# Kernel optimization log

Measured on AMD Instinct MI355X. Metric: run time of the kernel, lower is better.

## Reference

```python
import jax, jax.numpy as jnp
import numpy as np

N, E, S, K, NB = 16384, 262144, 10, 64, 8
R_MAX, P_CUT, AVG_NEIGH = 5.0, 5, 16.0
L_OF_LM = np.array([0, 1, 1, 1, 2, 2, 2, 2, 2])  # l value of each of the 9 lm components
L_SLICES = [(0, 1), (1, 4), (4, 9)]               # lm ranges for l = 0,1,2
MLP_H = 16


def _sph(u):
    # real spherical harmonics up to l=2, e3nn 'component' normalization (sum_m Y_lm^2 = 2l+1)
    x, y, z = u[..., 0], u[..., 1], u[..., 2]
    s3, s15, s5 = np.float32(np.sqrt(3.0)), np.float32(np.sqrt(15.0)), np.float32(np.sqrt(5.0))
    return jnp.stack([
        jnp.ones_like(x),
        s3 * x, s3 * y, s3 * z,
        s15 * x * y, s15 * y * z, (s5 / 2) * (3 * z * z - 1), s15 * x * z, (s15 / 2) * (x * x - y * y),
    ], axis=-1)


def _radial(r):
    # Bessel radial basis with smooth polynomial cutoff envelope (p = P_CUT)
    u = r / R_MAX
    r_safe = jnp.where(r > 1e-9, r, 1.0)
    n = jnp.arange(1, NB + 1, dtype=r.dtype)
    bess = np.float32(np.sqrt(2.0 / R_MAX)) * jnp.sin(n * jnp.pi * u[:, None]) / r_safe[:, None]
    p = float(P_CUT)
    env = 1.0 - (p + 1) * (p + 2) / 2 * u**P_CUT + p * (p + 2) * u**(P_CUT + 1) - p * (p + 1) / 2 * u**(P_CUT + 2)
    env = jnp.where(u < 1.0, env, 0.0)
    return bess * env[:, None]  # [E, NB]


def setup_inputs() -> dict:
    key = jax.random.key(0)
    ks = jax.random.split(key, 16)
    positions = jax.random.uniform(ks[0], (N, 3), jnp.float32) * 4.0  # box so many edges fall inside r_max
    species = jax.random.randint(ks[1], (N,), 0, S)
    senders = jax.random.randint(ks[2], (E,), 0, N)
    receivers = jax.random.randint(ks[3], (E,), 0, N)
    shifts = jnp.zeros((E, 3), jnp.float32)
    W_embed = jax.random.normal(ks[4], (S, K), jnp.float32)
    W_rad = jax.random.normal(ks[5], (2, 3, NB, K), jnp.float32) * 0.3
    W_mix = jax.random.normal(ks[6], (2, 3, K, K), jnp.float32) / np.sqrt(K)
    W_prod = jax.random.normal(ks[7], (2, 3, 3, K), jnp.float32) * 0.1
    W_sc = jax.random.normal(ks[8], (2, S, 3, K, K), jnp.float32) / np.sqrt(K)
    W_ro0 = jax.random.normal(ks[9], (K,), jnp.float32) / np.sqrt(K)
    W_m1 = jax.random.normal(ks[10], (K, MLP_H), jnp.float32) / np.sqrt(K)
    b_m1 = jnp.zeros((MLP_H,), jnp.float32)
    W_m2 = jax.random.normal(ks[11], (MLP_H,), jnp.float32) / np.sqrt(MLP_H)
    return dict(positions=positions, shifts=shifts, species=species, senders=senders,
                receivers=receivers, W_embed=W_embed, W_rad=W_rad, W_mix=W_mix,
                W_prod=W_prod, W_sc=W_sc, W_ro0=W_ro0, W_m1=W_m1, b_m1=b_m1, W_m2=W_m2)


def reference(positions, shifts, species, senders, receivers, W_embed, W_rad, W_mix,
              W_prod, W_sc, W_ro0, W_m1, b_m1, W_m2):
    lm = jnp.asarray(L_OF_LM)
    onehot = jax.nn.one_hot(species, S, dtype=positions.dtype)
    # node embedding: scalars only -> feats [N, 9(lm), K]
    feats = jnp.zeros((N, 9, K), positions.dtype).at[:, 0, :].set(onehot @ W_embed)

    # edge geometry
    vec = positions[receivers] - positions[senders] + shifts           # [E, 3]
    r = jnp.linalg.norm(vec, axis=-1)                                  # [E]
    u_hat = vec / jnp.where(r > 1e-9, r, 1.0)[:, None]
    Y = _sph(u_hat)                                                     # [E, 9]
    rad = _radial(r)                                                    # [E, NB]

    energies = []
    for i in range(2):
        # interaction: radial-weighted SH messages from sender scalars, scatter-sum to receivers
        hs = feats[:, 0, :][senders]                                    # [E, K]
        Rl = jnp.einsum('eb,lbk->elk', rad, W_rad[i])[:, lm, :]         # [E, 9, K]
        msg = hs[:, None, :] * Y[:, :, None] * Rl                       # [E, 9, K]
        A = jax.ops.segment_sum(msg, receivers, num_segments=N) / AVG_NEIGH
        A = jnp.einsum('nmk,mkj->nmj', A, W_mix[i][lm])                 # per-l channel mixing

        # correlation-3 equivariant product basis (symmetric-contraction style)
        A0 = A[:, 0, :]
        inv = jnp.sum(A * A, axis=1)                                    # rotation-invariant [N, K]
        w1, w2, w3 = (W_prod[i, j][lm] for j in range(3))               # each [9, K]
        B = A * (w1[None] + w2[None] * A0[:, None, :] + w3[None] * inv[:, None, :])

        # species-dependent self-connection (linear of feats x node_attrs), per-l weights
        sc = jnp.concatenate([
            jnp.einsum('nmk,ns,skj->nmj', feats[:, st:en], onehot, W_sc[i, :, l])
            for l, (st, en) in enumerate(L_SLICES)], axis=1)
        feats = B + sc

        if i == 0:
            energies.append(feats[:, 0, :] @ W_ro0)                     # linear readout
        else:
            feats = feats.at[:, 1:, :].set(0.0)                         # last layer keeps 0e only
            energies.append(jax.nn.silu(feats[:, 0, :] @ W_m1 + b_m1) @ W_m2)

    return jnp.stack(energies, axis=1)  # [N, num_interactions]
```

## Files before the change

### kernel.cpp

```cpp
#include <hip/hip_runtime.h>

#define NN 16384
#define NE 262144
#define NSPEC 10
#define KC 64
#define MLPH 16
#define SEG 128
#define EPSG 2048
#define SC_NPB 16

typedef float v2f __attribute__((ext_vector_type(2)));

__device__ __forceinline__ float wave_reduce(float v) {
#pragma unroll
    for (int off = 32; off > 0; off >>= 1) v += __shfl_down(v, off, 64);
    return v;
}

__device__ __forceinline__ float f4c(const float4& v, int j) {
    const float* p = &v.x;
    return p[j];
}

__global__ void __launch_bounds__(1024) k_pre(
    const float* __restrict__ W_embed,
    const int* __restrict__ species,
    const int* __restrict__ receivers,
    int* __restrict__ eslot,
    unsigned short* __restrict__ cnt16,
    float4* __restrict__ h04) {
    __shared__ int cntL[NN];
    int t = threadIdx.x;
#pragma unroll
    for (int i = 0; i < 16; ++i) cntL[t + 1024 * i] = 0;
    __syncthreads();
    int ebase = blockIdx.x * EPSG;
#pragma unroll
    for (int j = 0; j < EPSG / 1024; ++j) {
        int e = ebase + j * 1024 + t;
        int r = receivers[e];
        eslot[e] = atomicAdd(&cntL[r], 1);
    }
    int gt = blockIdx.x * 1024 + t;
#pragma unroll
    for (int q = 0; q < 2; ++q) {
        int idx = gt * 2 + q;
        int n = idx >> 4, w = idx & 15;
        h04[idx] = reinterpret_cast<const float4*>(W_embed + species[n] * KC)[w];
    }
    __syncthreads();
    unsigned short* o = cnt16 + (size_t)blockIdx.x * NN;
#pragma unroll
    for (int i = 0; i < 16; ++i)
        o[t + 1024 * i] = (unsigned short)cntL[t + 1024 * i];
}

__global__ void __launch_bounds__(128) k_colscan(
    const unsigned short* __restrict__ cnt16,
    int* __restrict__ seg_base,
    int* __restrict__ count) {
    int r = blockIdx.x * 128 + threadIdx.x;
    int run = 0;
#pragma unroll 8
    for (int g = 0; g < SEG; ++g) {
        int c = cnt16[(size_t)g * NN + r];
        seg_base[(size_t)g * NN + r] = run;
        run += c;
    }
    count[r] = run;
}

__global__ void __launch_bounds__(1024) k_scan(
    const int* __restrict__ count, int* __restrict__ row_start,
    const int* __restrict__ species, int* __restrict__ nslot,
    int* __restrict__ sp_start) {
    __shared__ int lds[1024];
    __shared__ int itercnt[256 * NSPEC];
    __shared__ int spt[NSPEC];
    int t = threadIdx.x;
    int lane = t & 63;
    int w = t >> 6;
#pragma unroll
    for (int j = 0; j < 16; ++j) {
        int n = w * 1024 + j * 64 + lane;
        int sp = species[n];
#pragma unroll
        for (int s = 0; s < NSPEC; ++s) {
            unsigned long long mask = __ballot(sp == s);
            if (lane == 0) itercnt[(w * 16 + j) * NSPEC + s] = (int)__popcll(mask);
        }
    }
    int base = t * 16;
    int local[16];
    int ssum = 0;
#pragma unroll
    for (int b = 0; b < 16; ++b) { local[b] = count[base + b]; ssum += local[b]; }
    lds[t] = ssum;
    __syncthreads();
    for (int off = 1; off < 1024; off <<= 1) {
        int v = (t >= off) ? lds[t - off] : 0;
        __syncthreads();
        lds[t] += v;
        __syncthreads();
    }
    int run = lds[t] - ssum;
#pragma unroll
    for (int b = 0; b < 16; ++b) { row_start[base + b] = run; run += local[b]; }
    if (t == 1023) row_start[NN] = run;
    __syncthreads();
    if (w < NSPEC) {
        int s = w;
        int v0 = itercnt[(lane * 4 + 0) * NSPEC + s];
        int v1 = itercnt[(lane * 4 + 1) * NSPEC + s];
        int v2 = itercnt[(lane * 4 + 2) * NSPEC + s];
        int v3 = itercnt[(lane * 4 + 3) * NSPEC + s];
        int ls = v0 + v1 + v2 + v3;
        int inc = ls;
#pragma unroll
        for (int off = 1; off < 64; off <<= 1) {
            int v = __shfl_up(inc, off, 64);
            if (lane >= off) inc += v;
        }
        int exc = inc - ls;
        itercnt[(lane * 4 + 0) * NSPEC + s] = exc;
        itercnt[(lane * 4 + 1) * NSPEC + s] = exc + v0;
        itercnt[(lane * 4 + 2) * NSPEC + s] = exc + v0 + v1;
        itercnt[(lane * 4 + 3) * NSPEC + s] = exc + v0 + v1 + v2;
        if (lane == 63) spt[s] = inc;
    }
    __syncthreads();
    if (t == 0) {
        int r2 = 0;
        for (int s = 0; s < NSPEC; ++s) { sp_start[s] = r2; r2 += spt[s]; }
        sp_start[NSPEC] = r2;
    }
    __syncthreads();
#pragma unroll
    for (int j = 0; j < 16; ++j) {
        int n = w * 1024 + j * 64 + lane;
        int sp = species[n];
        int rank = 0;
#pragma unroll
        for (int s = 0; s < NSPEC; ++s) {
            unsigned long long mask = __ballot(sp == s);
            if (sp == s)
                rank = (int)__popcll(mask & ((1ull << lane) - 1ull));
        }
        nslot[n] = itercnt[(w * 16 + j) * NSPEC + sp] + rank;
    }
}

__global__ void k_geom(const float* __restrict__ pos,
                       const float* __restrict__ shifts,
                       const int* __restrict__ senders,
                       const int* __restrict__ receivers,
                       const int* __restrict__ row_start,
                       const int* __restrict__ seg_base,
                       const int* __restrict__ eslot,
                       const int* __restrict__ species,
                       const int* __restrict__ sp_start,
                       const int* __restrict__ nslot,
                       int* __restrict__ ord,
                       float* __restrict__ edgerec,
                       int* __restrict__ ssend) {
    int e = blockIdx.x * 256 + threadIdx.x;
    if (e < NN) {
        int sp = species[e];
        ord[sp_start[sp] + nslot[e]] = e;
    }
    int s = senders[e], r = receivers[e];
    float dx = pos[r * 3 + 0] - pos[s * 3 + 0] + shifts[e * 3 + 0];
    float dy = pos[r * 3 + 1] - pos[s * 3 + 1] + shifts[e * 3 + 1];
    float dz = pos[r * 3 + 2] - pos[s * 3 + 2] + shifts[e * 3 + 2];
    float rn = sqrtf(dx * dx + dy * dy + dz * dz);
    float den = (rn > 1e-9f) ? rn : 1.0f;
    float x = dx / den, y = dy / den, z = dz / den;
    const float s3  = 1.7320508075688772f;
    const float s15 = 3.8729833462074170f;
    const float s5h = 1.1180339887498949f;
    const float s15h = 1.9364916731037085f;
    float rec[16];
    rec[0] = s3 * x;
    rec[1] = s3 * y;
    rec[2] = s3 * z;
    rec[3] = s15 * x * y;
    rec[4] = s15 * y * z;
    rec[5] = s5h * (3.0f * z * z - 1.0f);
    rec[6] = s15 * x * z;
    rec[7] = s15h * (x * x - y * y);
    float u = rn * 0.2f;
    float env = 0.0f;
    if (u < 1.0f) {
        float u2 = u * u;
        float u5 = u2 * u2 * u;
        env = 1.0f - 21.0f * u5 + 35.0f * u5 * u - 15.0f * u5 * u2;
    }
    float pre = 0.63245553203367587f * env / den;
    float half_u = 0.5f * u;
#pragma unroll
    for (int nb = 1; nb <= 8; ++nb) {
        float tr = (float)nb * half_u;
        tr -= floorf(tr);
        rec[7 + nb] = pre * __builtin_amdgcn_sinf(tr);
    }
    int p = row_start[r] + seg_base[(size_t)(e >> 11) * NN + r] + eslot[e];
    float4* o = (float4*)(edgerec + (size_t)p * 16);
#pragma unroll
    for (int i = 0; i < 4; ++i)
        o[i] = make_float4(rec[4 * i], rec[4 * i + 1], rec[4 * i + 2], rec[4 * i + 3]);
    ssend[p] = s;
}

__device__ __forceinline__ void agg_edge_pk(
    const float* __restrict__ rc, float hv,
    const float (&Wr0)[8], const v2f (&Wr12)[8],
    float& acc0, v2f (&accp)[4]) {
    float R0 = 0.f;
    v2f R12 = (v2f){0.f, 0.f};
#pragma unroll
    for (int b = 0; b < 8; ++b) {
        float rb = rc[8 + b];
        R0 = fmaf(rb, Wr0[b], R0);
        R12 = __builtin_elementwise_fma((v2f){rb, rb}, Wr12[b], R12);
    }
    acc0 = fmaf(hv, R0, acc0);
    float t1 = hv * R12.x, t2 = hv * R12.y;
    accp[0] = __builtin_elementwise_fma((v2f){t1, t1}, (v2f){rc[0], rc[1]}, accp[0]);
    accp[1] = __builtin_elementwise_fma((v2f){t1, t2}, (v2f){rc[2], rc[3]}, accp[1]);
    accp[2] = __builtin_elementwise_fma((v2f){t2, t2}, (v2f){rc[4], rc[5]}, accp[2]);
    accp[3] = __builtin_elementwise_fma((v2f){t2, t2}, (v2f){rc[6], rc[7]}, accp[3]);
}

__global__ void __launch_bounds__(512, 8) k_aggmix(
    const float* __restrict__ h,
    const float* __restrict__ edgerec,
    const int* __restrict__ ssend,
    const int* __restrict__ row_start,
    const float* __restrict__ Wr_i,
    const float* __restrict__ Wm_i,
    const float* __restrict__ Wp_i,
    float* __restrict__ Bm0) {
    __shared__ float Wlds[4096];
    __shared__ float xtile[8][9 * 64];
    {
        float4* Wl4 = (float4*)Wlds;
        const float4* W4 = (const float4*)(Wm_i + 2 * 4096);
#pragma unroll
        for (int i = 0; i < 2; ++i)
            Wl4[threadIdx.x + 512 * i] = W4[threadIdx.x + 512 * i];
    }
    __syncthreads();
    int lane = threadIdx.x & 63;
    int wid = __builtin_amdgcn_readfirstlane(threadIdx.x >> 6);
    float* xt = xtile[wid];
    float Wr0[8];
    v2f  Wr12[8];
#pragma unroll
    for (int b = 0; b < 8; ++b) {
        Wr0[b]    = Wr_i[b * 64 + lane] * (1.0f / 16.0f);
        Wr12[b].x = Wr_i[(8 + b) * 64 + lane] * (1.0f / 16.0f);
        Wr12[b].y = Wr_i[(16 + b) * 64 + lane] * (1.0f / 16.0f);
    }
    float w10 = Wp_i[0 * 64 + lane];
    float w20 = Wp_i[3 * 64 + lane];
    float w30 = Wp_i[6 * 64 + lane];
    const float* W0g = Wm_i;
    const float* W1g = Wm_i + 4096;

    int nA = (blockIdx.x * 8 + wid) * 2;
    int nB = nA + 1;
    int eA0 = row_start[nA], eA1 = row_start[nA + 1], eB1 = row_start[nB + 1];
    int eB0 = eA1;
    int cA = eA1 - eA0, cB = eB1 - eB0;
    int mc = min(cA, cB);

    float accA0 = 0.f, accB0 = 0.f;
    v2f accAp[4], accBp[4];
#pragma unroll
    for (int q = 0; q < 4; ++q) { accAp[q] = (v2f){0.f, 0.f}; accBp[q] = (v2f){0.f, 0.f}; }

#pragma unroll 2
    for (int i = 0; i < mc; ++i) {
        int ea = eA0 + i, eb = eB0 + i;
        int sa = ssend[ea], sb = ssend[eb];
        float ha = h[(size_t)sa * 64 + lane];
        float hb = h[(size_t)sb * 64 + lane];
        const float* ra = edgerec + (size_t)ea * 16;
        const float* rb = edgerec + (size_t)eb * 16;
        agg_edge_pk(ra, ha, Wr0, Wr12, accA0, accAp);
        agg_edge_pk(rb, hb, Wr0, Wr12, accB0, accBp);
    }
#pragma unroll 2
    for (int i = mc; i < cA; ++i) {
        int ea = eA0 + i;
        int sa = ssend[ea];
        float ha = h[(size_t)sa * 64 + lane];
        agg_edge_pk(edgerec + (size_t)ea * 16, ha, Wr0, Wr12, accA0, accAp);
    }
#pragma unroll 2
    for (int i = mc; i < cB; ++i) {
        int eb = eB0 + i;
        int sb = ssend[eb];
        float hb = h[(size_t)sb * 64 + lane];
        agg_edge_pk(edgerec + (size_t)eb * 16, hb, Wr0, Wr12, accB0, accBp);
    }

#pragma unroll
    for (int nn = 0; nn < 2; ++nn) {
        float a0 = nn ? accB0 : accA0;
        v2f* ap = nn ? accBp : accAp;
        int n = nn ? nB : nA;
        xt[0 * 64 + lane] = a0;
        xt[1 * 64 + lane] = ap[0].x;  xt[2 * 64 + lane] = ap[0].y;
        xt[3 * 64 + lane] = ap[1].x;  xt[4 * 64 + lane] = ap[1].y;
        xt[5 * 64 + lane] = ap[2].x;  xt[6 * 64 + lane] = ap[2].y;
        xt[7 * 64 + lane] = ap[3].x;  xt[8 * 64 + lane] = ap[3].y;
        v2f mixp[9];
#pragma unroll
        for (int m = 0; m < 9; ++m) mixp[m] = (v2f){0.f, 0.f};
#pragma unroll 2
        for (int c4 = 0; c4 < 16; ++c4) {
            float4 xb[9];
#pragma unroll
            for (int m = 0; m < 9; ++m)
                xb[m] = *(const float4*)&xt[m * 64 + c4 * 4];
#pragma unroll
            for (int j2 = 0; j2 < 2; ++j2) {
                int k0 = c4 * 4 + j2 * 2;
                v2f wv0 = (v2f){W0g[k0 * 64 + lane], W0g[(k0 + 1) * 64 + lane]};
                v2f wv1 = (v2f){W1g[k0 * 64 + lane], W1g[(k0 + 1) * 64 + lane]};
                v2f wv2 = (v2f){Wlds[k0 * 64 + lane], Wlds[(k0 + 1) * 64 + lane]};
#pragma unroll
                for (int m = 0; m < 9; ++m) {
                    v2f xp = (v2f){f4c(xb[m], j2 * 2), f4c(xb[m], j2 * 2 + 1)};
                    v2f wv = (m == 0) ? wv0 : ((m < 4) ? wv1 : wv2);
                    mixp[m] = __builtin_elementwise_fma(xp, wv, mixp[m]);
                }
            }
        }
        float mix[9];
#pragma unroll
        for (int m = 0; m < 9; ++m) mix[m] = mixp[m].x + mixp[m].y;
        float A0 = mix[0];
        float inv = 0.f;
#pragma unroll
        for (int m = 0; m < 9; ++m) inv += mix[m] * mix[m];
        Bm0[(size_t)n * 64 + lane] = mix[0] * (w10 + w20 * A0 + w30 * inv);
    }
}

template <int ITER>
__global__ void __launch_bounds__(256) k_sc(
    const float* __restrict__ h_in,
    const float* __restrict__ Bm0,
    float* __restrict__ h_out,
    const int* __restrict__ ord,
    const int* __restrict__ species,
    const float* __restrict__ Wsc_i,
    const float* __restrict__ W_ro0,
    const float* __restrict__ W_m1,
    const float* __restrict__ b_m1,
    const float* __restrict__ W_m2,
    float* __restrict__ out) {
    __shared__ float Wlds[4096];
    __shared__ float xtile[4][4 * 64];
    int idx0 = blockIdx.x * SC_NPB;
    int s0 = species[ord[idx0]];
    {
        const float4* W4 = (const float4*)(Wsc_i + (size_t)s0 * 3 * 4096);
        float4* Wl4 = (float4*)Wlds;
#pragma unroll
        for (int i = 0; i < 4; ++i)
            Wl4[threadIdx.x + 256 * i] = W4[threadIdx.x + 256 * i];
    }
    __syncthreads();
    int lane = threadIdx.x & 63;
    int wid = threadIdx.x >> 6;
    float* xt = xtile[wid];
    int q0 = idx0 + wid * 4;
    int nd[4];
#pragma unroll
    for (int t = 0; t < 4; ++t) nd[t] = ord[q0 + t];
    float xv[4];
#pragma unroll
    for (int t = 0; t < 4; ++t) xv[t] = h_in[(size_t)nd[t] * 64 + lane];
#pragma unroll
    for (int t = 0; t < 4; ++t) xt[t * 64 + lane] = xv[t];
    float acc[4] = {0.f, 0.f, 0.f, 0.f};
#pragma unroll 4
    for (int c4 = 0; c4 < 16; ++c4) {
        float wv[4];
#pragma unroll
        for (int j = 0; j < 4; ++j) wv[j] = Wlds[(c4 * 4 + j) * 64 + lane];
#pragma unroll
        for (int t = 0; t < 4; ++t) {
            float4 xb = *(const float4*)&xt[t * 64 + c4 * 4];
#pragma unroll
            for (int j = 0; j < 4; ++j) acc[t] += f4c(xb, j) * wv[j];
        }
    }
#pragma unroll
    for (int t = 0; t < 4; ++t) {
        int spt = species[nd[t]];
        if (spt != s0) {
            const float* Wg = Wsc_i + (size_t)spt * 3 * 4096;
            float a = 0.f;
            for (int k = 0; k < 64; ++k)
                a += xt[t * 64 + k] * Wg[k * 64 + lane];
            acc[t] = a;
        }
    }
    float wro = W_ro0[lane];
#pragma unroll
    for (int t = 0; t < 4; ++t) {
        int node = nd[t];
        float outv = acc[t] + Bm0[(size_t)node * 64 + lane];
        if (ITER == 0) {
            h_out[(size_t)node * 64 + lane] = outv;
            float e = wave_reduce(outv * wro);
            if (lane == 0) out[2 * node + 0] = e;
        } else {
            int hh = lane & 15;
            float tacc = b_m1[hh];
#pragma unroll
            for (int k = 0; k < 64; ++k)
                tacc += __shfl(outv, k, 64) * W_m1[k * MLPH + hh];
            float sig = 1.0f / (1.0f + expf(-tacc));
            float contrib = (lane < MLPH) ? tacc * sig * W_m2[lane] : 0.f;
            float e = wave_reduce(contrib);
            if (lane == 0) out[2 * node + 1] = e;
        }
    }
}

extern "C" void kernel_launch(void* const* d_in, const int* in_sizes, int n_in,
                              void* d_out, int out_size, void* d_ws, size_t ws_size,
                              hipStream_t stream) {
    const float* positions = (const float*)d_in[0];
    const float* shifts    = (const float*)d_in[1];
    const int*   species   = (const int*)d_in[2];
    const int*   senders   = (const int*)d_in[3];
    const int*   receivers = (const int*)d_in[4];
    const float* W_embed   = (const float*)d_in[5];
    const float* W_rad     = (const float*)d_in[6];
    const float* W_mix     = (const float*)d_in[7];
    const float* W_prod    = (const float*)d_in[8];
    const float* W_sc      = (const float*)d_in[9];
    const float* W_ro0     = (const float*)d_in[10];
    const float* W_m1      = (const float*)d_in[11];
    const float* b_m1      = (const float*)d_in[12];
    const float* W_m2      = (const float*)d_in[13];
    float* out = (float*)d_out;

    char* p = (char*)d_ws;
    float* edgerec = (float*)p; p += (size_t)NE * 16 * 4;
    int* seg_base  = (int*)p;   p += (size_t)SEG * NN * 4;
    float* Bm0     = (float*)p; p += (size_t)NN * KC * 4;
    float* h0      = (float*)p; p += (size_t)NN * KC * 4;
    float* h1      = (float*)p; p += (size_t)NN * KC * 4;
    unsigned short* cnt16 = (unsigned short*)p; p += (size_t)SEG * NN * 2;
    int* eslot     = (int*)p; p += (size_t)NE * 4;
    int* ssend     = (int*)p; p += (size_t)NE * 4;
    int* nslot     = (int*)p; p += (size_t)NN * 4;
    int* ord       = (int*)p; p += (size_t)NN * 4;
    int* count     = (int*)p; p += (size_t)NN * 4;
    int* row_start = (int*)p; p += (size_t)(NN + 1) * 4;
    int* sp_start  = (int*)p; p += 16 * 4;

    k_pre<<<SEG, 1024, 0, stream>>>(W_embed, species, receivers,
                                    eslot, cnt16, (float4*)h0);
    k_colscan<<<NN / 128, 128, 0, stream>>>(cnt16, seg_base, count);
    k_scan<<<1, 1024, 0, stream>>>(count, row_start, species, nslot, sp_start);
    k_geom<<<NE / 256, 256, 0, stream>>>(positions, shifts, senders, receivers,
                                         row_start, seg_base, eslot, species,
                                         sp_start, nslot, ord, edgerec, ssend);

    k_aggmix<<<NN / 16, 512, 0, stream>>>(h0, edgerec, ssend, row_start,
        W_rad + 0, W_mix + 0, W_prod + 0, Bm0);
    k_sc<0><<<NN / SC_NPB, 256, 0, stream>>>(h0, Bm0, h1, ord, species,
        W_sc + 0, W_ro0, W_m1, b_m1, W_m2, out);

    k_aggmix<<<NN / 16, 512, 0, stream>>>(h1, edgerec, ssend, row_start,
        W_rad + 1536, W_mix + 12288, W_prod + 576, Bm0);
    k_sc<1><<<NN / SC_NPB, 256, 0, stream>>>(h1, Bm0, h0 , ord, species,
        W_sc + (size_t)NSPEC * 3 * 4096, W_ro0, W_m1, b_m1, W_m2, out);
}
```

Before: 264.8 us.

## Stage edge records in LDS per 4-edge group and shuffle sender indices

The aggregation loop now loads the sender indices of up to 64 edges per node in a single coalesced lane-parallel read and broadcasts them with wave shuffles. It also copies each group of four 16-float edge records into LDS with one coalesced load per wave, instead of every lane reading the same record through uniform global loads. The aim is to cut redundant scalar and broadcast global traffic in the edge loop. In exchange it adds LDS traffic, shuffles, and per-group branching, and it uses the xt scratch buffer without any barrier; that is only safe if xt is private to the wave.

```diff
diff --git a/kernel.cpp b/kernel.cpp
--- a/kernel.cpp
+++ b/kernel.cpp
@@ -212,7 +212,7 @@
 }
 
 __device__ __forceinline__ void agg_edge_pk(
-    const float* __restrict__ rc, float hv,
+    const float* rc, float hv,
     const float (&Wr0)[8], const v2f (&Wr12)[8],
     float& acc0, v2f (&accp)[4]) {
     float R0 = 0.f;
@@ -272,37 +272,54 @@
     int eA0 = row_start[nA], eA1 = row_start[nA + 1], eB1 = row_start[nB + 1];
     int eB0 = eA1;
     int cA = eA1 - eA0, cB = eB1 - eB0;
-    int mc = min(cA, cB);
+
+    int sAllA = ssend[cA ? min(eA0 + lane, eA1 - 1) : 0];
+    int sAllB = ssend[cB ? min(eB0 + lane, eB1 - 1) : 0];
 
     float accA0 = 0.f, accB0 = 0.f;
     v2f accAp[4], accBp[4];
 #pragma unroll
     for (int q = 0; q < 4; ++q) { accAp[q] = (v2f){0.f, 0.f}; accBp[q] = (v2f){0.f, 0.f}; }
 
-#pragma unroll 2
-    for (int i = 0; i < mc; ++i) {
-        int ea = eA0 + i, eb = eB0 + i;
-        int sa = ssend[ea], sb = ssend[eb];
-        float ha = h[(size_t)sa * 64 + lane];
-        float hb = h[(size_t)sb * 64 + lane];
-        const float* ra = edgerec + (size_t)ea * 16;
-        const float* rb = edgerec + (size_t)eb * 16;
-        agg_edge_pk(ra, ha, Wr0, Wr12, accA0, accAp);
-        agg_edge_pk(rb, hb, Wr0, Wr12, accB0, accBp);
-    }
-#pragma unroll 2
-    for (int i = mc; i < cA; ++i) {
-        int ea = eA0 + i;
-        int sa = ssend[ea];
-        float ha = h[(size_t)sa * 64 + lane];
-        agg_edge_pk(edgerec + (size_t)ea * 16, ha, Wr0, Wr12, accA0, accAp);
-    }
-#pragma unroll 2
-    for (int i = mc; i < cB; ++i) {
-        int eb = eB0 + i;
-        int sb = ssend[eb];
-        float hb = h[(size_t)sb * 64 + lane];
-        agg_edge_pk(edgerec + (size_t)eb * 16, hb, Wr0, Wr12, accB0, accBp);
+    int ngA = (cA + 3) >> 2, ngB = (cB + 3) >> 2;
+    int ng = max(ngA, ngB);
+    for (int gg = 0; gg < ng; ++gg) {
+        int baseA = eA0 + gg * 4, baseB = eB0 + gg * 4;
+        int remA = eA1 - baseA; remA = (remA < 0) ? 0 : ((remA > 4) ? 4 : remA);
+        int remB = eB1 - baseB; remB = (remB < 0) ? 0 : ((remB > 4) ? 4 : remB);
+        if (remA > 0) {
+            int src = min(baseA * 16 + lane, eA1 * 16 - 1);
+            xt[lane] = edgerec[src];
+        }
+        if (remB > 0) {
+            int src = min(baseB * 16 + lane, eB1 * 16 - 1);
+            xt[64 + lane] = edgerec[src];
+        }
+        int rm = min(remA, remB);
+#pragma unroll 4
+        for (int i = 0; i < rm; ++i) {
+            int idx = gg * 4 + i;
+            int sa = (idx < 64) ? __shfl(sAllA, idx, 64) : ssend[baseA + i];
+            int sb = (idx < 64) ? __shfl(sAllB, idx, 64) : ssend[baseB + i];
+            float ha = h[(size_t)sa * 64 + lane];
+            float hb = h[(size_t)sb * 64 + lane];
+            agg_edge_pk(xt + 16 * i, ha, Wr0, Wr12, accA0, accAp);
+            agg_edge_pk(xt + 64 + 16 * i, hb, Wr0, Wr12, accB0, accBp);
+        }
+#pragma unroll 4
+        for (int i = rm; i < remA; ++i) {
+            int idx = gg * 4 + i;
+            int sa = (idx < 64) ? __shfl(sAllA, idx, 64) : ssend[baseA + i];
+            float ha = h[(size_t)sa * 64 + lane];
+            agg_edge_pk(xt + 16 * i, ha, Wr0, Wr12, accA0, accAp);
+        }
+#pragma unroll 4
+        for (int i = rm; i < remB; ++i) {
+            int idx = gg * 4 + i;
+            int sb = (idx < 64) ? __shfl(sAllB, idx, 64) : ssend[baseB + i];
+            float hb = h[(size_t)sb * 64 + lane];
+            agg_edge_pk(xt + 64 + 16 * i, hb, Wr0, Wr12, accB0, accBp);
+        }
     }
 
 #pragma unroll
```

Result: slower. 433.4 us (+63.7%).

## Move species ranking into k_pre and use wave-shuffle scan in k_scan

Applied to the files above, without the earlier changes.

Per-64-node species ranks and chunk counts are now computed in parallel in k_pre (the first 16 blocks), not by the single-block k_scan. k_scan's 1024-thread Hillis-Steele LDS scan with many barriers is replaced by a two-level wave shuffle scan. It then only scans the precomputed chunk counts into per-chunk bases, which k_geom adds when building the species order. This shortens the serial single-block scan kernel, at the cost of an extra global buffer and one extra lookup per node in k_geom.

```diff
diff --git a/kernel.cpp b/kernel.cpp
--- a/kernel.cpp
+++ b/kernel.cpp
@@ -7,6 +7,7 @@
 #define MLPH 16
 #define SEG 128
 #define EPSG 2048
+#define NCHUNK 256
 #define SC_NPB 16
 
 typedef float v2f __attribute__((ext_vector_type(2)));
@@ -28,9 +29,12 @@
     const int* __restrict__ receivers,
     int* __restrict__ eslot,
     unsigned short* __restrict__ cnt16,
+    int* __restrict__ nslot,
+    int* __restrict__ chunkcnt,
     float4* __restrict__ h04) {
     __shared__ int cntL[NN];
     int t = threadIdx.x;
+    int lane = t & 63;
 #pragma unroll
     for (int i = 0; i < 16; ++i) cntL[t + 1024 * i] = 0;
     __syncthreads();
@@ -41,7 +45,20 @@
         int r = receivers[e];
         eslot[e] = atomicAdd(&cntL[r], 1);
     }
-    int gt = blockIdx.x * 1024 + t;
+    int tid = blockIdx.x * 1024 + t;
+    if (tid < NN) {
+        int sp = species[tid];
+        int rank = 0, mycnt = 0;
+#pragma unroll
+        for (int s = 0; s < NSPEC; ++s) {
+            unsigned long long mask = __ballot(sp == s);
+            if (sp == s) rank = (int)__popcll(mask & ((1ull << lane) - 1ull));
+            if (lane == s) mycnt = (int)__popcll(mask);
+        }
+        nslot[tid] = rank;
+        if (lane < NSPEC) chunkcnt[(tid >> 6) * NSPEC + lane] = mycnt;
+    }
+    int gt = tid;
 #pragma unroll
     for (int q = 0; q < 2; ++q) {
         int idx = gt * 2 + q;
@@ -72,81 +89,67 @@
 
 __global__ void __launch_bounds__(1024) k_scan(
     const int* __restrict__ count, int* __restrict__ row_start,
-    const int* __restrict__ species, int* __restrict__ nslot,
+    const int* __restrict__ chunkcnt,
+    int* __restrict__ cbase,
     int* __restrict__ sp_start) {
-    __shared__ int lds[1024];
-    __shared__ int itercnt[256 * NSPEC];
+    __shared__ int wsum[16];
     __shared__ int spt[NSPEC];
     int t = threadIdx.x;
     int lane = t & 63;
     int w = t >> 6;
-#pragma unroll
-    for (int j = 0; j < 16; ++j) {
-        int n = w * 1024 + j * 64 + lane;
-        int sp = species[n];
-#pragma unroll
-        for (int s = 0; s < NSPEC; ++s) {
-            unsigned long long mask = __ballot(sp == s);
-            if (lane == 0) itercnt[(w * 16 + j) * NSPEC + s] = (int)__popcll(mask);
-        }
-    }
     int base = t * 16;
     int local[16];
     int ssum = 0;
 #pragma unroll
     for (int b = 0; b < 16; ++b) { local[b] = count[base + b]; ssum += local[b]; }
-    lds[t] = ssum;
-    __syncthreads();
-    for (int off = 1; off < 1024; off <<= 1) {
-        int v = (t >= off) ? lds[t - off] : 0;
-        __syncthreads();
-        lds[t] += v;
-        __syncthreads();
-    }
-    int run = lds[t] - ssum;
+    int inc = ssum;
+#pragma unroll
+    for (int off = 1; off < 64; off <<= 1) {
+        int v = __shfl_up(inc, off, 64);
+        if (lane >= off) inc += v;
+    }
+    if (lane == 63) wsum[w] = inc;
+    __syncthreads();
+    if (w == 0) {
+        int v = (lane < 16) ? wsum[lane] : 0;
+        int inc2 = v;
+#pragma unroll
+        for (int off = 1; off < 16; off <<= 1) {
+            int u = __shfl_up(inc2, off, 64);
+            if (lane >= off) inc2 += u;
+        }
+        if (lane < 16) wsum[lane] = inc2 - v;
+    }
+    __syncthreads();
+    int run = wsum[w] + (inc - ssum);
 #pragma unroll
     for (int b = 0; b < 16; ++b) { row_start[base + b] = run; run += local[b]; }
     if (t == 1023) row_start[NN] = run;
-    __syncthreads();
     if (w < NSPEC) {
         int s = w;
-        int v0 = itercnt[(lane * 4 + 0) * NSPEC + s];
-        int v1 = itercnt[(lane * 4 + 1) * NSPEC + s];
-        int v2 = itercnt[(lane * 4 + 2) * NSPEC + s];
-        int v3 = itercnt[(lane * 4 + 3) * NSPEC + s];
+        int v0 = chunkcnt[(lane * 4 + 0) * NSPEC + s];
+        int v1 = chunkcnt[(lane * 4 + 1) * NSPEC + s];
+        int v2 = chunkcnt[(lane * 4 + 2) * NSPEC + s];
+        int v3 = chunkcnt[(lane * 4 + 3) * NSPEC + s];
         int ls = v0 + v1 + v2 + v3;
-        int inc = ls;
+        int inc3 = ls;
 #pragma unroll
         for (int off = 1; off < 64; off <<= 1) {
-            int v = __shfl_up(inc, off, 64);
-            if (lane >= off) inc += v;
-        }
-        int exc = inc - ls;
-        itercnt[(lane * 4 + 0) * NSPEC + s] = exc;
-        itercnt[(lane * 4 + 1) * NSPEC + s] = exc + v0;
-        itercnt[(lane * 4 + 2) * NSPEC + s] = exc + v0 + v1;
-        itercnt[(lane * 4 + 3) * NSPEC + s] = exc + v0 + v1 + v2;
-        if (lane == 63) spt[s] = inc;
+            int v = __shfl_up(inc3, off, 64);
+            if (lane >= off) inc3 += v;
+        }
+        int exc = inc3 - ls;
+        cbase[(lane * 4 + 0) * NSPEC + s] = exc;
+        cbase[(lane * 4 + 1) * NSPEC + s] = exc + v0;
+        cbase[(lane * 4 + 2) * NSPEC + s] = exc + v0 + v1;
+        cbase[(lane * 4 + 3) * NSPEC + s] = exc + v0 + v1 + v2;
+        if (lane == 63) spt[s] = inc3;
     }
     __syncthreads();
     if (t == 0) {
         int r2 = 0;
         for (int s = 0; s < NSPEC; ++s) { sp_start[s] = r2; r2 += spt[s]; }
         sp_start[NSPEC] = r2;
-    }
-    __syncthreads();
-#pragma unroll
-    for (int j = 0; j < 16; ++j) {
-        int n = w * 1024 + j * 64 + lane;
-        int sp = species[n];
-        int rank = 0;
-#pragma unroll
-        for (int s = 0; s < NSPEC; ++s) {
-            unsigned long long mask = __ballot(sp == s);
-            if (sp == s)
-                rank = (int)__popcll(mask & ((1ull << lane) - 1ull));
-        }
-        nslot[n] = itercnt[(w * 16 + j) * NSPEC + sp] + rank;
     }
 }
 
@@ -159,6 +162,7 @@
                        const int* __restrict__ eslot,
                        const int* __restrict__ species,
                        const int* __restrict__ sp_start,
+                       const int* __restrict__ cbase,
                        const int* __restrict__ nslot,
                        int* __restrict__ ord,
                        float* __restrict__ edgerec,
@@ -166,7 +170,7 @@
     int e = blockIdx.x * 256 + threadIdx.x;
     if (e < NN) {
         int sp = species[e];
-        ord[sp_start[sp] + nslot[e]] = e;
+        ord[sp_start[sp] + cbase[(e >> 6) * NSPEC + sp] + nslot[e]] = e;
     }
     int s = senders[e], r = receivers[e];
     float dx = pos[r * 3 + 0] - pos[s * 3 + 0] + shifts[e * 3 + 0];
@@ -465,15 +469,18 @@
     int* ord       = (int*)p; p += (size_t)NN * 4;
     int* count     = (int*)p; p += (size_t)NN * 4;
     int* row_start = (int*)p; p += (size_t)(NN + 1) * 4;
+    int* chunkcnt  = (int*)p; p += (size_t)NCHUNK * NSPEC * 4;
+    int* cbase     = (int*)p; p += (size_t)NCHUNK * NSPEC * 4;
     int* sp_start  = (int*)p; p += 16 * 4;
 
     k_pre<<<SEG, 1024, 0, stream>>>(W_embed, species, receivers,
-                                    eslot, cnt16, (float4*)h0);
+                                    eslot, cnt16, nslot, chunkcnt, (float4*)h0);
     k_colscan<<<NN / 128, 128, 0, stream>>>(cnt16, seg_base, count);
-    k_scan<<<1, 1024, 0, stream>>>(count, row_start, species, nslot, sp_start);
+    k_scan<<<1, 1024, 0, stream>>>(count, row_start, chunkcnt, cbase, sp_start);
     k_geom<<<NE / 256, 256, 0, stream>>>(positions, shifts, senders, receivers,
                                          row_start, seg_base, eslot, species,
-                                         sp_start, nslot, ord, edgerec, ssend);
+                                         sp_start, cbase, nslot, ord,
+                                         edgerec, ssend);
 
     k_aggmix<<<NN / 16, 512, 0, stream>>>(h0, edgerec, ssend, row_start,
         W_rad + 0, W_mix + 0, W_prod + 0, Bm0);
```

Result: faster. 250.7 us (-5.3%).
